# Kernel tuning notes

Measured on AMD Instinct MI355X. Metric: run time of the kernel, lower is better.

Reference implementation:

```python
import jax, jax.numpy as jnp
import numpy as np

N, D, M = 50000, 6, 32  # particles, state_dim, num_measurements
MD = 3                  # measurement dim (rho, alpha, epsilon)
_LOG2PI = jnp.log(2.0 * jnp.pi)


def h(x):
    # Radar measurement of a single state: uses position = x[:3]
    px, py, pz = x[0], x[1], x[2]
    rho = jnp.sqrt(px * px + py * py + pz * pz)
    return jnp.stack([rho, jnp.arctan2(py, px), jnp.arcsin(pz / rho)])


def setup_inputs() -> dict:
    key = jax.random.key(0)
    k1, k2, k3, k4 = jax.random.split(key, 4)
    scale = jnp.array([1000.0, 1000.0, 1000.0, 10.0, 10.0, 10.0], dtype=jnp.float32)
    offset = jnp.array([5000.0, 5000.0, 5000.0, 0.0, 0.0, 0.0], dtype=jnp.float32)
    means = jax.random.normal(k1, (N, D), dtype=jnp.float32) * scale + offset
    covs = jax.random.normal(k2, (N, D, D), dtype=jnp.float32)  # only used for zeros_like shape
    weights = jax.random.uniform(k3, (N,), dtype=jnp.float32)
    noise_std = jnp.array([1.0, jnp.deg2rad(0.5), jnp.deg2rad(0.5)], dtype=jnp.float32)
    measurements = jax.vmap(h)(means[:M]) + jax.random.normal(k4, (M, MD), dtype=jnp.float32) * noise_std
    measurements_mask = jnp.ones((M,), dtype=bool)
    R = jnp.diag(noise_std ** 2)  # measurement_system.covariance
    return {"means": means, "covs": covs, "weights": weights,
            "measurements": measurements, "measurements_mask": measurements_mask, "R": R}


def reference(means, covs, weights, measurements, measurements_mask, R):
    n, d = means.shape
    m = measurements.shape[0]
    md = measurements.shape[1]

    # Silverman-style bandwidth and localized empirical covariance (shared across particles)
    bandwidth = (4.0 / (n * (d + 2))) ** (2.0 / (d + 4))
    Xc = means - jnp.mean(means, axis=0)
    emp = (Xc.T @ Xc) / (n - 1)  # jnp.cov(means.T), ddof=1
    idx = jnp.arange(d)
    dist = jnp.abs(idx[:, None] - idx[None, :]).astype(means.dtype)
    rho_loc = jnp.exp(-dist ** 2 / (2.0 * 3.0 ** 2))  # L = 3.0
    P = bandwidth * (emp * rho_loc)  # [d, d] mixture covariance

    # Per-particle autodiff Jacobian of the measurement function (as in update_point)
    H = jax.vmap(jax.jacfwd(h))(means)                     # [N, md, d]
    S = jnp.einsum('nij,jk,nlk->nil', H, P, H) + R          # [N, md, md] innovation cov
    Sinv = jnp.linalg.inv(S)
    K = jnp.einsum('ij,nkj,nkl->nil', P, H, Sinv)           # [N, d, md] Kalman gain
    I = jnp.eye(d, dtype=means.dtype)
    KH = jnp.einsum('nik,nkj->nij', K, H)
    covs_post = jnp.einsum('nij,jk->nik', I - KH, P)        # [N, d, d]

    # Updated points per (measurement, particle)
    hx = jax.vmap(h)(means)                                 # [N, md]
    innov = hx[None, :, :] - measurements[:, None, :]       # [M, N, md] = h(x) - z
    pts = means[None, :, :] - jnp.einsum('ndk,mnk->mnd', K, innov)  # [M, N, d]

    # logpdf of measurement under N(h(updated point), S)
    h_post = jax.vmap(jax.vmap(h))(pts)                     # [M, N, md]
    diff = measurements[:, None, :] - h_post                # [M, N, md]
    L = jnp.linalg.cholesky(S)                              # [N, md, md]
    Lb = jnp.broadcast_to(L[None], (m, n, md, md))
    y = jax.scipy.linalg.solve_triangular(Lb, diff[..., None], lower=True)[..., 0]
    quad = jnp.sum(y * y, axis=-1)                          # [M, N]
    logdet = jnp.sum(jnp.log(jnp.diagonal(L, axis1=-2, axis2=-1)), axis=-1)  # [N]
    logw = -0.5 * quad - logdet[None, :] - 0.5 * md * _LOG2PI  # [M, N]

    # lax.cond on measurements_mask -> masked select of zeros / -inf
    mask = measurements_mask
    pts = jnp.where(mask[:, None, None], pts, jnp.zeros_like(means)[None])
    logw = jnp.where(mask[:, None], logw, -jnp.inf)
    covs_out = jnp.where(mask[:, None, None, None],
                         jnp.broadcast_to(covs_post[None], (m, n, d, d)),
                         jnp.zeros_like(covs)[None])
    return pts, logw, covs_out
```

## Files before the change

kernel.cpp:

```cpp
#include <hip/hip_runtime.h>
#include <math.h>


#define NDIM 6
#define MDIM 3
#define NB_STATS 128
#define MSPLIT 8
#define GROUP_M 4
typedef float f32x4 __attribute__((ext_vector_type(4)));

__device__ __forceinline__ bool mask_true(const int* m32, const unsigned char* m8, int m) {
    return (m32[m] != 0) || (m8[m] != 0);
}

__global__ __launch_bounds__(256) void stats_partial_kernel(const float* __restrict__ means,
                                                            int N, double* __restrict__ partials) {
    double sx[6];
    double sxx[21];
#pragma unroll
    for (int i = 0; i < 6; ++i) sx[i] = 0.0;
#pragma unroll
    for (int i = 0; i < 21; ++i) sxx[i] = 0.0;

    int stride = NB_STATS * 256;
    for (int n = blockIdx.x * 256 + threadIdx.x; n < N; n += stride) {
        const float2* mp = (const float2*)(means + (size_t)n * 6);
        float2 a = mp[0], b = mp[1], c = mp[2];
        double x[6] = {a.x, a.y, b.x, b.y, c.x, c.y};
        int p = 0;
#pragma unroll
        for (int i = 0; i < 6; ++i) {
            sx[i] += x[i];
#pragma unroll
            for (int j = i; j < 6; ++j) sxx[p++] += x[i] * x[j];
        }
    }
#pragma unroll
    for (int off = 32; off >= 1; off >>= 1) {
#pragma unroll
        for (int i = 0; i < 6; ++i) sx[i] += __shfl_down(sx[i], off);
#pragma unroll
        for (int i = 0; i < 21; ++i) sxx[i] += __shfl_down(sxx[i], off);
    }
    __shared__ double lds[4][27];
    int wave = threadIdx.x >> 6;
    if ((threadIdx.x & 63) == 0) {
#pragma unroll
        for (int i = 0; i < 6; ++i) lds[wave][i] = sx[i];
#pragma unroll
        for (int i = 0; i < 21; ++i) lds[wave][6 + i] = sxx[i];
    }
    __syncthreads();
    if (threadIdx.x < 27) {
        double v = lds[0][threadIdx.x] + lds[1][threadIdx.x] +
                   lds[2][threadIdx.x] + lds[3][threadIdx.x];
        partials[threadIdx.x * NB_STATS + blockIdx.x] = v;
    }
}

__device__ __forceinline__ void build_P_block(const double* __restrict__ partials, int N,
                                              double* __restrict__ sStats,
                                              double* __restrict__ sP,
                                              float* __restrict__ sPf) {
    if (threadIdx.x < 27) {
        const double* src = partials + (size_t)threadIdx.x * NB_STATS;
        double acc = 0.0;
#pragma unroll 8
        for (int b = 0; b < NB_STATS; ++b) acc += src[b];
        sStats[threadIdx.x] = acc;
    }
    __syncthreads();
    if (threadIdx.x == 0) {
        double mean[6];
#pragma unroll
        for (int i = 0; i < 6; ++i) mean[i] = sStats[i] / (double)N;
        double bandwidth = pow(4.0 / ((double)N * 8.0), 0.2);
        int p = 0;
        for (int i = 0; i < 6; ++i) {
            for (int j = i; j < 6; ++j) {
                double emp = (sStats[6 + p] - (double)N * mean[i] * mean[j]) / (double)(N - 1);
                double dd = (double)(j - i);
                double val = bandwidth * emp * exp(-(dd * dd) / 18.0);
                sP[i * 6 + j] = val;
                sP[j * 6 + i] = val;
                ++p;
            }
        }
    }
    __syncthreads();
    if (threadIdx.x < 36) sPf[threadIdx.x] = (float)sP[threadIdx.x];
    __syncthreads();
}

struct PData {
    float hx0, hx1, hx2, logdet;
    float L00, L10, L11, L20, L21, L22;
    float Kf[6][3];
    float H[3][3];
};

__device__ __forceinline__ void particle_compute(const float* __restrict__ means,
                                                 const float* __restrict__ Rin,
                                                 const double* __restrict__ sP,
                                                 int n, float* __restrict__ x, PData& o) {
    const float2* mp = (const float2*)(means + (size_t)n * 6);
    float2 ma = mp[0], mb = mp[1], mc = mp[2];
    x[0] = ma.x; x[1] = ma.y; x[2] = mb.x; x[3] = mb.y; x[4] = mc.x; x[5] = mc.y;
    float px = ma.x, py = ma.y, pz = mb.x;
    float s2 = px * px + py * py;
    float r2 = s2 + pz * pz;
    float rho = sqrtf(r2);
    float s = sqrtf(s2);
    o.hx0 = rho;
    o.hx1 = atan2f(py, px);
    o.hx2 = asinf(pz / rho);
    o.H[0][0] = px / rho; o.H[0][1] = py / rho; o.H[0][2] = pz / rho;
    o.H[1][0] = -py / s2; o.H[1][1] = px / s2;  o.H[1][2] = 0.0f;
    float invr2s = 1.0f / (r2 * s);
    o.H[2][0] = -pz * px * invr2s; o.H[2][1] = -pz * py * invr2s; o.H[2][2] = s / r2;

    double T[3][3];
#pragma unroll
    for (int i = 0; i < 3; ++i)
#pragma unroll
        for (int k = 0; k < 3; ++k)
            T[i][k] = (double)o.H[i][0] * sP[0 * 6 + k] + (double)o.H[i][1] * sP[1 * 6 + k] +
                      (double)o.H[i][2] * sP[2 * 6 + k];
    double S[3][3];
#pragma unroll
    for (int i = 0; i < 3; ++i)
#pragma unroll
        for (int l = 0; l < 3; ++l)
            S[i][l] = T[i][0] * (double)o.H[l][0] + T[i][1] * (double)o.H[l][1] +
                      T[i][2] * (double)o.H[l][2] + (double)Rin[i * 3 + l];

    double L00 = sqrt(S[0][0]);
    double L10 = S[1][0] / L00;
    double L20 = S[2][0] / L00;
    double L11 = sqrt(S[1][1] - L10 * L10);
    double L21 = (S[2][1] - L20 * L10) / L11;
    double L22 = sqrt(S[2][2] - L20 * L20 - L21 * L21);
    o.L00 = (float)L00; o.L10 = (float)L10; o.L11 = (float)L11;
    o.L20 = (float)L20; o.L21 = (float)L21; o.L22 = (float)L22;
    o.logdet = logf((float)(L00 * L11 * L22));

    double a00 = S[0][0], a01 = S[0][1], a02 = S[0][2];
    double a11 = S[1][1], a12 = S[1][2], a22 = S[2][2];
    double c00 = a11 * a22 - a12 * a12;
    double c01 = a02 * a12 - a01 * a22;
    double c02 = a01 * a12 - a02 * a11;
    double c11 = a00 * a22 - a02 * a02;
    double c12 = a01 * a02 - a00 * a12;
    double c22 = a00 * a11 - a01 * a01;
    double invdet = 1.0 / (a00 * c00 + a01 * c01 + a02 * c02);
    double Si[3][3] = {{c00 * invdet, c01 * invdet, c02 * invdet},
                       {c01 * invdet, c11 * invdet, c12 * invdet},
                       {c02 * invdet, c12 * invdet, c22 * invdet}};

#pragma unroll
    for (int i = 0; i < 6; ++i) {
        double pht[3];
#pragma unroll
        for (int k = 0; k < 3; ++k)
            pht[k] = sP[i * 6 + 0] * (double)o.H[k][0] + sP[i * 6 + 1] * (double)o.H[k][1] +
                     sP[i * 6 + 2] * (double)o.H[k][2];
#pragma unroll
        for (int l = 0; l < 3; ++l)
            o.Kf[i][l] = (float)(pht[0] * Si[0][l] + pht[1] * Si[1][l] + pht[2] * Si[2][l]);
    }
}

__global__ __launch_bounds__(256) void fused_all_kernel(const float* __restrict__ means,
                                                        const float* __restrict__ meas,
                                                        const int* __restrict__ mask32,
                                                        const unsigned char* __restrict__ mask8,
                                                        const float* __restrict__ Rin,
                                                        const double* __restrict__ partials,
                                                        float* __restrict__ pts,
                                                        float* __restrict__ logw,
                                                        float* __restrict__ covs,
                                                        int N, int M, int CB, int UBx) {
    __shared__ double sStats[27];
    __shared__ double sP[36];
    __shared__ float sPf[36];
    __shared__ float sbuf[256 * 36];

    build_P_block(partials, N, sStats, sP, sPf);

    int b = blockIdx.x;
    int tid = threadIdx.x;

    if (b < CB) {
        int nb = b / MSPLIT;
        int g = b - nb * MSPLIT;
        int n0 = nb * 256;
        int count = N - n0;
        if (count > 256) count = 256;

        if (tid < count) {
            float x[6];
            PData o;
            particle_compute(means, Rin, sP, n0 + tid, x, o);
            float KH[6][3];
#pragma unroll
            for (int i = 0; i < 6; ++i)
#pragma unroll
                for (int j = 0; j < 3; ++j)
                    KH[i][j] = o.Kf[i][0] * o.H[0][j] + o.Kf[i][1] * o.H[1][j] +
                               o.Kf[i][2] * o.H[2][j];
            float* row = sbuf + tid * 36;
#pragma unroll
            for (int i = 0; i < 6; ++i)
#pragma unroll
                for (int j = 0; j < 6; ++j)
                    row[i * 6 + j] = sPf[i * 6 + j] - (KH[i][0] * sPf[0 * 6 + j] +
                                                       KH[i][1] * sPf[1 * 6 + j] +
                                                       KH[i][2] * sPf[2 * 6 + j]);
        }
        __syncthreads();

        int nf4 = count * 9;
        const f32x4* s4 = (const f32x4*)sbuf;
        f32x4 z = {0.f, 0.f, 0.f, 0.f};
        for (int m = g; m < M; m += MSPLIT) {
            bool mk = mask_true(mask32, mask8, m);
            f32x4* d4 = (f32x4*)covs + ((size_t)m * N + n0) * 9;
            if (mk) {
                for (int i = tid; i < nf4; i += 256) d4[i] = s4[i];
            } else {
                for (int i = tid; i < nf4; i += 256) d4[i] = z;
            }
        }
        return;
    }

    int u = b - CB;
    int mg = u / UBx;
    int nb = u - mg * UBx;
    int n0 = nb * 256;
    int count = N - n0;
    if (count > 256) count = 256;

    float x[6];
    PData o;
    if (tid < count) particle_compute(means, Rin, sP, n0 + tid, x, o);

#pragma unroll
    for (int j = 0; j < GROUP_M; ++j) {
        int m = mg * GROUP_M + j;
        if (m >= M) break;
        bool mk = mask_true(mask32, mask8, m);
        __syncthreads();
        if (tid < count) {
            float pt[6];
            if (mk) {
                float z0 = meas[m * 3 + 0];
                float z1 = meas[m * 3 + 1];
                float z2v = meas[m * 3 + 2];
                float i0 = o.hx0 - z0, i1 = o.hx1 - z1, i2 = o.hx2 - z2v;
#pragma unroll
                for (int d = 0; d < 6; ++d)
                    pt[d] = x[d] - (o.Kf[d][0] * i0 + o.Kf[d][1] * i1 + o.Kf[d][2] * i2);
                float px = pt[0], py = pt[1], pz = pt[2];
                float r2 = px * px + py * py + pz * pz;
                float rho = sqrtf(r2);
                float d0 = z0 - rho;
                float d1 = z1 - atan2f(py, px);
                float d2 = z2v - asinf(pz / rho);
                float y0 = d0 / o.L00;
                float y1 = (d1 - o.L10 * y0) / o.L11;
                float y2 = (d2 - o.L20 * y0 - o.L21 * y1) / o.L22;
                float quad = y0 * y0 + y1 * y1 + y2 * y2;
                logw[(size_t)m * N + n0 + tid] = -0.5f * quad - o.logdet - 2.7568156f;
            } else {
#pragma unroll
                for (int d = 0; d < 6; ++d) pt[d] = 0.f;
                logw[(size_t)m * N + n0 + tid] = -INFINITY;
            }
#pragma unroll
            for (int d = 0; d < 6; ++d) sbuf[tid * 6 + d] = pt[d];
        }
        __syncthreads();
        int nf = count * 6;
        float* dst = pts + ((size_t)m * N + n0) * 6;
        const f32x4* s4 = (const f32x4*)sbuf;
        f32x4* d4 = (f32x4*)dst;
        int n4 = nf >> 2;
        for (int i = tid; i < n4; i += 256) d4[i] = s4[i];
        for (int i = (n4 << 2) + tid; i < nf; i += 256) dst[i] = sbuf[i];
    }
}

extern "C" void kernel_launch(void* const* d_in, const int* in_sizes, int n_in,
                              void* d_out, int out_size, void* d_ws, size_t ws_size,
                              hipStream_t stream) {
    const float* means = (const float*)d_in[0];
    const float* meas = (const float*)d_in[3];
    const int* mask32 = (const int*)d_in[4];
    const unsigned char* mask8 = (const unsigned char*)d_in[4];
    const float* Rin = (const float*)d_in[5];

    int N = in_sizes[0] / NDIM;
    int M = in_sizes[3] / MDIM;

    float* out = (float*)d_out;
    float* pts = out;
    float* logw = out + (size_t)M * N * 6;
    float* covs = out + (size_t)M * N * 7;

    double* partials = (double*)d_ws;

    int UBx = (N + 255) / 256;
    int MG = (M + GROUP_M - 1) / GROUP_M;
    int CB = UBx * MSPLIT;
    int UB = UBx * MG;

    stats_partial_kernel<<<NB_STATS, 256, 0, stream>>>(means, N, partials);
    fused_all_kernel<<<CB + UB, 256, 0, stream>>>(means, meas, mask32, mask8, Rin,
                                                  partials, pts, logw, covs, N, M, CB, UBx);
}
```

Measured before the change: 78.74 us.

## Compute mixture covariance once in separate kernel and shrink covariance chunk size

Moves the reduction of per-block statistics and construction of P out of every block of the fused kernel into a dedicated single-block kernel, so each fused block only loads 36 precomputed doubles. The reduction itself is parallelised across 8 lanes per statistic. The covariance-writing blocks now handle 128 particles instead of 256, halving LDS use and doubling the number of such blocks, but the code shown still stages only the first 128 threads. This adds an extra kernel launch in exchange for removing redundant per-block serial work.

```diff
diff --git a/kernel.cpp b/kernel.cpp
--- a/kernel.cpp
+++ b/kernel.cpp
@@ -7,6 +7,7 @@
 #define NB_STATS 128
 #define MSPLIT 8
 #define GROUP_M 4
+#define CHUNK 128
 typedef float f32x4 __attribute__((ext_vector_type(4)));
 
 __device__ __forceinline__ bool mask_true(const int* m32, const unsigned char* m8, int m) {
@@ -58,38 +59,43 @@
     }
 }
 
-__device__ __forceinline__ void build_P_block(const double* __restrict__ partials, int N,
-                                              double* __restrict__ sStats,
-                                              double* __restrict__ sP,
-                                              float* __restrict__ sPf) {
-    if (threadIdx.x < 27) {
-        const double* src = partials + (size_t)threadIdx.x * NB_STATS;
+__global__ __launch_bounds__(256) void computeP_kernel(const double* __restrict__ partials,
+                                                       int N, double* __restrict__ P64) {
+    __shared__ double red[27][8];
+    int tid = threadIdx.x;
+    int s = tid >> 3, j = tid & 7;
+    if (s < 27) {
+        const double* src = partials + (size_t)s * NB_STATS + j * 16;
         double acc = 0.0;
-#pragma unroll 8
-        for (int b = 0; b < NB_STATS; ++b) acc += src[b];
-        sStats[threadIdx.x] = acc;
+#pragma unroll
+        for (int k = 0; k < 16; ++k) acc += src[k];
+        red[s][j] = acc;
     }
     __syncthreads();
-    if (threadIdx.x == 0) {
+    if (tid < 27) {
+        double a = 0.0;
+#pragma unroll
+        for (int q = 0; q < 8; ++q) a += red[tid][q];
+        red[tid][0] = a;
+    }
+    __syncthreads();
+    if (tid == 0) {
         double mean[6];
 #pragma unroll
-        for (int i = 0; i < 6; ++i) mean[i] = sStats[i] / (double)N;
+        for (int i = 0; i < 6; ++i) mean[i] = red[i][0] / (double)N;
         double bandwidth = pow(4.0 / ((double)N * 8.0), 0.2);
         int p = 0;
         for (int i = 0; i < 6; ++i) {
-            for (int j = i; j < 6; ++j) {
-                double emp = (sStats[6 + p] - (double)N * mean[i] * mean[j]) / (double)(N - 1);
-                double dd = (double)(j - i);
+            for (int jj = i; jj < 6; ++jj) {
+                double emp = (red[6 + p][0] - (double)N * mean[i] * mean[jj]) / (double)(N - 1);
+                double dd = (double)(jj - i);
                 double val = bandwidth * emp * exp(-(dd * dd) / 18.0);
-                sP[i * 6 + j] = val;
-                sP[j * 6 + i] = val;
+                P64[i * 6 + jj] = val;
+                P64[jj * 6 + i] = val;
                 ++p;
             }
         }
     }
-    __syncthreads();
-    if (threadIdx.x < 36) sPf[threadIdx.x] = (float)sP[threadIdx.x];
-    __syncthreads();
 }
 
 struct PData {
@@ -175,27 +181,31 @@
                                                         const int* __restrict__ mask32,
                                                         const unsigned char* __restrict__ mask8,
                                                         const float* __restrict__ Rin,
-                                                        const double* __restrict__ partials,
+                                                        const double* __restrict__ P64,
                                                         float* __restrict__ pts,
                                                         float* __restrict__ logw,
                                                         float* __restrict__ covs,
                                                         int N, int M, int CB, int UBx) {
-    __shared__ double sStats[27];
     __shared__ double sP[36];
     __shared__ float sPf[36];
-    __shared__ float sbuf[256 * 36];
-
-    build_P_block(partials, N, sStats, sP, sPf);
+    __shared__ float sbuf[CHUNK * 36];
+
+    int tid = threadIdx.x;
+    if (tid < 36) {
+        double v = P64[tid];
+        sP[tid] = v;
+        sPf[tid] = (float)v;
+    }
+    __syncthreads();
 
     int b = blockIdx.x;
-    int tid = threadIdx.x;
 
     if (b < CB) {
-        int nb = b / MSPLIT;
-        int g = b - nb * MSPLIT;
-        int n0 = nb * 256;
+        int c = b / MSPLIT;
+        int g = b - c * MSPLIT;
+        int n0 = c * CHUNK;
         int count = N - n0;
-        if (count > 256) count = 256;
+        if (count > CHUNK) count = CHUNK;
 
         if (tid < count) {
             float x[6];
@@ -309,13 +319,16 @@
     float* covs = out + (size_t)M * N * 7;
 
     double* partials = (double*)d_ws;
+    double* P64 = partials + 27 * NB_STATS;
 
     int UBx = (N + 255) / 256;
     int MG = (M + GROUP_M - 1) / GROUP_M;
-    int CB = UBx * MSPLIT;
+    int NC = (N + CHUNK - 1) / CHUNK;
+    int CB = NC * MSPLIT;
     int UB = UBx * MG;
 
     stats_partial_kernel<<<NB_STATS, 256, 0, stream>>>(means, N, partials);
+    computeP_kernel<<<1, 256, 0, stream>>>(partials, N, P64);
     fused_all_kernel<<<CB + UB, 256, 0, stream>>>(means, meas, mask32, mask8, Rin,
-                                                  partials, pts, logw, covs, N, M, CB, UBx);
-}
+                                                  P64, pts, logw, covs, N, M, CB, UBx);
+}
```

After: 68.57 us. 1.15x faster.
